# Performance work log

Hardware: AMD Instinct MI355X
Metric: run time of the kernel (lower is better)

## Reference

```python
import jax, jax.numpy as jnp
import numpy as np

B, T, E = 2, 2048, 2048
H, HKV, M = 16, 4, 4
HD = E // H // M          # 32
NREP = H // HKV           # 4
EPS = 1e-5


def _rotary_interleaved(x, cos, sin):
    # x: (B, S, nh, HD); cos/sin: (S, HD//2), interleaved pairs (0::2, 1::2)
    x1 = x[..., 0::2]
    x2 = x[..., 1::2]
    c = cos[None, :, None, :]
    s = sin[None, :, None, :]
    o1 = x1 * c - x2 * s
    o2 = x1 * s + x2 * c
    return jnp.stack([o1, o2], axis=-1).reshape(x.shape)


def setup_inputs() -> dict:
    key = jax.random.key(0)
    ks = jax.random.split(key, 6)
    x = jax.random.normal(ks[0], (B, T, E), jnp.float32)
    pos = jnp.arange(T, dtype=jnp.float32)
    inv_freq = 1.0 / (10000.0 ** (jnp.arange(0, HD, 2, dtype=jnp.float32) / HD))
    ang = pos[:, None] * inv_freq[None, :]  # (T, HD//2)
    cos = jnp.cos(ang)
    sin = jnp.sin(ang)
    s = 0.02
    q_w = jax.random.normal(ks[1], (E, E), jnp.float32) * s
    k_w = jax.random.normal(ks[2], (E // NREP, E), jnp.float32) * s
    v_w = jax.random.normal(ks[3], (E // NREP, E), jnp.float32) * s
    out_w = jax.random.normal(ks[4], (E, E), jnp.float32) * s
    raw_map_weights = jnp.array([0.1 * (-1.0) ** i for i in range(M)], jnp.float32)
    weight_scale = jnp.ones((1,), jnp.float32)
    gamma = jnp.ones((M * HD,), jnp.float32)
    return dict(x=x, cos=cos, sin=sin, q_w=q_w, k_w=k_w, v_w=v_w, out_w=out_w,
                raw_map_weights=raw_map_weights, weight_scale=weight_scale, gamma=gamma)


def reference(x, cos, sin, q_w, k_w, v_w, out_w, raw_map_weights, weight_scale, gamma):
    # projections
    q = (x @ q_w.T).reshape(B, T, M * H, HD)
    k = (x @ k_w.T).reshape(B, T, M * HKV, HD)
    v = (x @ v_w.T).reshape(B, T, HKV, M * HD)
    # rotary (interleaved) on full head_dim, then split heads x maps (heads major, maps minor)
    q = _rotary_interleaved(q, cos, sin).reshape(B, T, H, M, HD)
    k = _rotary_interleaved(k, cos, sin).reshape(B, T, HKV, M, HD)
    # GQA: q head h attends to kv head h // NREP  (repeat_interleave semantics)
    k_rep = jnp.repeat(k, NREP, axis=2)  # (B,T,H,M,HD)
    v_rep = jnp.repeat(v, NREP, axis=2)  # (B,T,H,M*HD)
    map_w = jnp.tanh(raw_map_weights) * weight_scale[0]
    scale = HD ** -0.5  # flash_attn default softmax scale
    causal = jnp.tril(jnp.ones((T, T), dtype=bool))
    combined = jnp.zeros((B, T, H, M * HD), x.dtype)
    for i in range(M):  # small fixed num_maps loop
        scores = jnp.einsum('bqhd,bkhd->bhqk', q[:, :, :, i], k_rep[:, :, :, i]) * scale
        scores = jnp.where(causal[None, None], scores, -jnp.inf)
        p = jax.nn.softmax(scores, axis=-1)
        attn_i = jnp.einsum('bhqk,bkhe->bqhe', p, v_rep)  # (B,T,H,M*HD)
        combined = combined + map_w[i] * attn_i
    # RMSNorm over last dim (num_maps * head_dim) with affine weight
    var = jnp.mean(combined * combined, axis=-1, keepdims=True)
    normed = combined * jax.lax.rsqrt(var + EPS) * gamma
    out = normed.reshape(B, T, E) @ out_w.T
    return out
```

## Files before the change

### kernel.cpp

```cpp
#include <hip/hip_runtime.h>


typedef unsigned short u16;
typedef unsigned int u32;
typedef _Float16 f16;
typedef _Float16 f16x8 __attribute__((ext_vector_type(8)));
typedef float f32x4 __attribute__((ext_vector_type(4)));

#define B_ 2
#define T_ 2048
#define E_ 2048
#define H_ 16
#define HKV_ 4
#define M_ 4
#define HD_ 32
#define SCALE_Q 0.2550348873f

#define GLOAD_LDS(g, l)                                                   \
  __builtin_amdgcn_global_load_lds(                                       \
      (const __attribute__((address_space(1))) u32*)(g),                  \
      (__attribute__((address_space(3))) u32*)(l), 16, 0, 0)

__device__ __forceinline__ u16 f2h(float f) {
  f16 h = (f16)f;
  return __builtin_bit_cast(u16, h);
}

__global__ void cvt_all(const float* __restrict__ x, const float* __restrict__ qw,
                        const float* __restrict__ kw, const float* __restrict__ vw,
                        const float* __restrict__ ow, u16* __restrict__ xb,
                        u16* __restrict__ wcat, u16* __restrict__ wo16) {
  const float* src;
  u16* dst;
  int n4;
  switch (blockIdx.y) {
    case 0: src = x;  dst = xb;            n4 = 2097152; break;
    case 1: src = qw; dst = wcat;          n4 = 1048576; break;
    case 2: src = kw; dst = wcat + 4194304; n4 = 262144; break;
    case 3: src = vw; dst = wcat + 5242880; n4 = 262144; break;
    default: src = ow; dst = wo16;         n4 = 1048576; break;
  }
  int i = blockIdx.x * blockDim.x + threadIdx.x;
  if (i < n4) {
    float4 v = ((const float4*)src)[i];
    ushort4 o;
    o.x = f2h(v.x); o.y = f2h(v.y); o.z = f2h(v.z); o.w = f2h(v.w);
    ((ushort4*)dst)[i] = o;
  }
}

#define GEMM_CORE(A_, B_ptr, K_)                                              \
  for (int k0 = 0; k0 < (K_); k0 += 32) {                                     \
    _Pragma("unroll") for (int j = 0; j < 2; ++j) {                           \
      GLOAD_LDS(&(A_)[(size_t)(m0 + r0 + j * 64) * (K_) + k0 + c8],           \
                &As[tid * 8 + j * 2048]);                                     \
      GLOAD_LDS(&(B_ptr)[(size_t)(n0 + r0 + j * 64) * (K_) + k0 + c8],        \
                &Bs[tid * 8 + j * 2048]);                                     \
    }                                                                         \
    __syncthreads();                                                          \
    f16x8 af[4], bfr[4];                                                      \
    _Pragma("unroll") for (int mt = 0; mt < 4; ++mt)                          \
        af[mt] = *(const f16x8*)&As[(wm + mt * 16 + r) * 32 + g * 8];         \
    _Pragma("unroll") for (int nt = 0; nt < 4; ++nt)                          \
        bfr[nt] = *(const f16x8*)&Bs[(wn + nt * 16 + r) * 32 + g * 8];        \
    _Pragma("unroll") for (int mt = 0; mt < 4; ++mt)                          \
        _Pragma("unroll") for (int nt = 0; nt < 4; ++nt)                      \
            acc[mt][nt] = __builtin_amdgcn_mfma_f32_16x16x32_f16(             \
                af[mt], bfr[nt], acc[mt][nt], 0, 0, 0);                       \
    __syncthreads();                                                          \
  }

__global__ __launch_bounds__(256) void gemm_bt(const u16* __restrict__ A,
                                               const u16* __restrict__ Bm,
                                               float* __restrict__ C,
                                               int M, int N, int K) {
  __shared__ __align__(16) u16 As[128 * 32];
  __shared__ __align__(16) u16 Bs[128 * 32];
  const int tid = threadIdx.x;
  const int lane = tid & 63;
  const int wv = tid >> 6;
  const int g = lane >> 4;
  const int r = lane & 15;
  const int m0 = blockIdx.y * 128;
  const int n0 = blockIdx.x * 128;
  const int wm = (wv >> 1) * 64;
  const int wn = (wv & 1) * 64;
  f32x4 acc[4][4];
#pragma unroll
  for (int a = 0; a < 4; ++a)
#pragma unroll
    for (int b = 0; b < 4; ++b) acc[a][b] = (f32x4){0.f, 0.f, 0.f, 0.f};
  const int r0 = tid >> 2;
  const int c8 = (tid & 3) << 3;

  GEMM_CORE(A, Bm, K)

#pragma unroll
  for (int mt = 0; mt < 4; ++mt)
#pragma unroll
    for (int nt = 0; nt < 4; ++nt) {
      int row = m0 + wm + mt * 16 + g * 4;
      int col = n0 + wn + nt * 16 + r;
#pragma unroll
      for (int rr = 0; rr < 4; ++rr)
        C[(size_t)(row + rr) * N + col] = acc[mt][nt][rr];
    }
}

__global__ __launch_bounds__(256) void gemm_qkv_rope(
    const u16* __restrict__ A, const u16* __restrict__ Bm,
    const float* __restrict__ cosb, const float* __restrict__ sinb,
    u16* __restrict__ qp, u16* __restrict__ kp, u16* __restrict__ vtp) {
  __shared__ __align__(16) u16 As[128 * 32];
  __shared__ __align__(16) u16 Bs[128 * 32];
  const int tid = threadIdx.x;
  const int lane = tid & 63;
  const int wv = tid >> 6;
  const int g = lane >> 4;
  const int r = lane & 15;
  const int m0 = blockIdx.y * 128;
  const int n0 = blockIdx.x * 128;
  const int wm = (wv >> 1) * 64;
  const int wn = (wv & 1) * 64;
  f32x4 acc[4][4];
#pragma unroll
  for (int a = 0; a < 4; ++a)
#pragma unroll
    for (int b = 0; b < 4; ++b) acc[a][b] = (f32x4){0.f, 0.f, 0.f, 0.f};
  const int r0 = tid >> 2;
  const int c8 = (tid & 3) << 3;

  GEMM_CORE(A, Bm, 2048)

  const int b = m0 >> 11;
  const float signf = (r & 1) ? 1.f : -1.f;
  const int jb = r >> 1;

  if (n0 < 2048) {
#pragma unroll
    for (int mt = 0; mt < 4; ++mt) {
      int row = m0 + wm + mt * 16 + g * 4;
      int t0 = row & 2047;
#pragma unroll
      for (int rr = 0; rr < 4; ++rr) {
        int t = t0 + rr;
        float c0 = cosb[t * 16 + jb], s0 = sinb[t * 16 + jb];
        float c1 = cosb[t * 16 + 8 + jb], s1 = sinb[t * 16 + 8 + jb];
#pragma unroll
        for (int nt = 0; nt < 4; ++nt) {
          float xv = acc[mt][nt][rr];
          float pv = __shfl_xor(xv, 1, 64);
          float c = (nt & 1) ? c1 : c0;
          float s = (nt & 1) ? s1 : s0;
          float o = (xv * c + signf * pv * s) * SCALE_Q;
          int col = n0 + wn + nt * 16 + r;
          int hh = col >> 7, mm = (col >> 5) & 3, d = col & 31;
          qp[((((size_t)b * H_ + hh) * M_ + mm) * T_ + t) * HD_ + d] = f2h(o);
        }
      }
    }
  } else if (n0 < 2560) {
#pragma unroll
    for (int mt = 0; mt < 4; ++mt) {
      int row = m0 + wm + mt * 16 + g * 4;
      int t0 = row & 2047;
#pragma unroll
      for (int rr = 0; rr < 4; ++rr) {
        int t = t0 + rr;
        float c0 = cosb[t * 16 + jb], s0 = sinb[t * 16 + jb];
        float c1 = cosb[t * 16 + 8 + jb], s1 = sinb[t * 16 + 8 + jb];
#pragma unroll
        for (int nt = 0; nt < 4; ++nt) {
          float xv = acc[mt][nt][rr];
          float pv = __shfl_xor(xv, 1, 64);
          float c = (nt & 1) ? c1 : c0;
          float s = (nt & 1) ? s1 : s0;
          float o = xv * c + signf * pv * s;
          int col2 = n0 + wn + nt * 16 + r - 2048;
          int hh = col2 >> 7, mm = (col2 >> 5) & 3, d = col2 & 31;
          kp[((((size_t)b * HKV_ + hh) * M_ + mm) * T_ + t) * HD_ + d] = f2h(o);
        }
      }
    }
  } else {
#pragma unroll
    for (int mt = 0; mt < 4; ++mt) {
      int row = m0 + wm + mt * 16 + g * 4;
      int t0 = row & 2047;
#pragma unroll
      for (int nt = 0; nt < 4; ++nt) {
        int col3 = n0 + wn + nt * 16 + r - 2560;
        int hkv = col3 >> 7, e = col3 & 127;
        ushort4 w;
        w.x = f2h(acc[mt][nt][0]);
        w.y = f2h(acc[mt][nt][1]);
        w.z = f2h(acc[mt][nt][2]);
        w.w = f2h(acc[mt][nt][3]);
        *(ushort4*)&vtp[(((size_t)b * HKV_ + hkv) * 128 + e) * T_ + t0] = w;
      }
    }
  }
}

__global__ __launch_bounds__(256) void lstats_kernel(
    const u16* __restrict__ qp, const u16* __restrict__ kp,
    const float* __restrict__ rawW, const float* __restrict__ wscale,
    float* __restrict__ invw) {
  const int tid = threadIdx.x;
  const int lane = tid & 63;
  const int wv = tid >> 6;
  const int g = lane >> 4, r = lane & 15;
  const int h = blockIdx.y;
  const int b = blockIdx.z >> 2, e = blockIdx.z & 3;
  const int hkv = h >> 2;
  const int s0 = blockIdx.x * 4 + wv;

  const size_t qb = (((size_t)b * H_ + h) * M_ + e) * T_ * HD_;
  const size_t kb = (((size_t)b * HKV_ + hkv) * M_ + e) * T_ * HD_;
  const float mw = tanhf(rawW[e]) * wscale[0];

  for (int ps = 0; ps < 2; ++ps) {
    const int strip = ps ? 127 - s0 : s0;
    const int q0 = strip * 16;
    f16x8 qf = *(const f16x8*)&qp[qb + (size_t)(q0 + r) * HD_ + g * 8];
    float lacc[4] = {0.f, 0.f, 0.f, 0.f};

    for (int k0 = 0; k0 < q0 + 16; k0 += 64) {
      f32x4 s[4];
#pragma unroll
      for (int nt = 0; nt < 4; ++nt) {
        f16x8 kf = *(const f16x8*)&kp[kb + (size_t)(k0 + nt * 16 + r) * HD_ + g * 8];
        s[nt] = __builtin_amdgcn_mfma_f32_16x16x32_f16(qf, kf, (f32x4){0.f, 0.f, 0.f, 0.f}, 0, 0, 0);
      }
#pragma unroll
      for (int rr = 0; rr < 4; ++rr) {
        int row = q0 + g * 4 + rr;
#pragma unroll
        for (int nt = 0; nt < 4; ++nt) {
          int col = k0 + nt * 16 + r;
          float sv = (col <= row) ? s[nt][rr] : -1e30f;
          lacc[rr] += exp2f(sv);
        }
      }
    }
#pragma unroll
    for (int rr = 0; rr < 4; ++rr) {
      float l = lacc[rr];
#pragma unroll
      for (int off = 8; off >= 1; off >>= 1) l += __shfl_xor(l, off, 64);
      if (r == 0)
        invw[(((size_t)b * H_ + h) * M_ + e) * T_ + q0 + g * 4 + rr] = mw / l;
    }
  }
}

__global__ __launch_bounds__(256) void attn_kernel(
    const u16* __restrict__ qp, const u16* __restrict__ kp,
    const u16* __restrict__ vtp, const float* __restrict__ invw,
    const float* __restrict__ gamma, u16* __restrict__ normed) {
  __shared__ __align__(16) char smem[42240];
  u16* Ks = (u16*)smem;
  u16* Pc = (u16*)(smem + 32768);
  float* comb = (float*)smem;

  const int tid = threadIdx.x;
  const int lane = tid & 63;
  const int wv = tid >> 6;
  const int g = lane >> 4;
  const int r = lane & 15;
  const int h = blockIdx.y;
  const int b = blockIdx.z;
  const int hkv = h >> 2;

  const size_t qb = ((size_t)b * H_ + h) * M_ * T_ * HD_;
  const size_t kb = ((size_t)b * HKV_ + hkv) * M_ * T_ * HD_;
  const size_t vb = ((size_t)b * HKV_ + hkv) * 128 * (size_t)T_;

#define STAGE_KS(K0, DST)                                                     \
  {                                                                           \
    _Pragma("unroll") for (int j = 0; j < 4; ++j) {                           \
      int f = tid + j * 256;                                                  \
      int e_ = f >> 8, g2 = (f >> 6) & 3, kk = f & 63;                        \
      GLOAD_LDS(&kp[kb + ((size_t)e_ * T_ + (K0) + kk) * HD_ + g2 * 8],       \
                &(DST)[f * 8]);                                               \
    }                                                                         \
  }

  for (int ps = 0; ps < 2; ++ps) {
    const int q0 = (ps ? 31 - blockIdx.x : blockIdx.x) * 64;
    const int rq = q0 + wv * 16;

    f16x8 qf[4];
    float iw[4][4];
#pragma unroll
    for (int e = 0; e < 4; ++e) {
      qf[e] = *(const f16x8*)&qp[qb + ((size_t)e * T_ + rq + r) * HD_ + g * 8];
      const float* ivp = invw + (((size_t)b * H_ + h) * M_ + e) * T_;
#pragma unroll
      for (int rr = 0; rr < 4; ++rr) iw[e][rr] = ivp[rq + g * 4 + rr];
    }

    f32x4 acc[4][2];
#pragma unroll
    for (int mt = 0; mt < 4; ++mt)
#pragma unroll
      for (int v2 = 0; v2 < 2; ++v2) acc[mt][v2] = (f32x4){0.f, 0.f, 0.f, 0.f};

    __syncthreads();
    STAGE_KS(0, (u16*)smem);
    __syncthreads();

    const int niter = q0 / 64 + 1;
    for (int i = 0; i < niter; ++i) {
      const int k0 = i * 64;
      u16* kbuf = (u16*)smem + (size_t)(i & 1) * 8192;
      u16* knext = (u16*)smem + (size_t)((i + 1) & 1) * 8192;

      if (i + 1 < niter) STAGE_KS(k0 + 64, knext);

      f16x8 vf[2][2];
#pragma unroll
      for (int v2 = 0; v2 < 2; ++v2)
#pragma unroll
        for (int k2 = 0; k2 < 2; ++k2)
          vf[v2][k2] = *(const f16x8*)&vtp[vb + (size_t)(wv * 32 + v2 * 16 + r) * T_ + k0 + k2 * 32 + g * 8];

      float pc[4][4];
#pragma unroll
      for (int nt = 0; nt < 4; ++nt)
#pragma unroll
        for (int rr = 0; rr < 4; ++rr) pc[nt][rr] = 0.f;
      if (k0 <= rq + 15) {
        const bool need_mask = (k0 + 63 > rq);
#pragma unroll
        for (int e = 0; e < 4; ++e) {
          f32x4 s[4];
#pragma unroll
          for (int nt = 0; nt < 4; ++nt) {
            f16x8 kf = *(const f16x8*)&kbuf[e * 2048 + g * 512 + (nt * 16 + r) * 8];
            s[nt] = __builtin_amdgcn_mfma_f32_16x16x32_f16(qf[e], kf, (f32x4){0.f, 0.f, 0.f, 0.f}, 0, 0, 0);
          }
#pragma unroll
          for (int nt = 0; nt < 4; ++nt)
#pragma unroll
            for (int rr = 0; rr < 4; ++rr) {
              float sv = s[nt][rr];
              if (need_mask && (k0 + nt * 16 + r > rq + g * 4 + rr)) sv = -1e30f;
              pc[nt][rr] = fmaf(exp2f(sv), iw[e][rr], pc[nt][rr]);
            }
        }
      }

      __syncthreads();

#pragma unroll
      for (int nt = 0; nt < 4; ++nt)
#pragma unroll
        for (int rr = 0; rr < 4; ++rr)
          Pc[(wv * 16 + g * 4 + rr) * 72 + nt * 16 + r] = f2h(pc[nt][rr]);

      __syncthreads();

#pragma unroll
      for (int mt = 0; mt < 4; ++mt) {
        f16x8 pf0 = *(const f16x8*)&Pc[(mt * 16 + r) * 72 + g * 8];
        f16x8 pf1 = *(const f16x8*)&Pc[(mt * 16 + r) * 72 + 32 + g * 8];
#pragma unroll
        for (int v2 = 0; v2 < 2; ++v2) {
          acc[mt][v2] = __builtin_amdgcn_mfma_f32_16x16x32_f16(pf0, vf[v2][0], acc[mt][v2], 0, 0, 0);
          acc[mt][v2] = __builtin_amdgcn_mfma_f32_16x16x32_f16(pf1, vf[v2][1], acc[mt][v2], 0, 0, 0);
        }
      }
    }

    __syncthreads();
#pragma unroll
    for (int mt = 0; mt < 4; ++mt)
#pragma unroll
      for (int v2 = 0; v2 < 2; ++v2)
#pragma unroll
        for (int rr = 0; rr < 4; ++rr)
          comb[(mt * 16 + g * 4 + rr) * 132 + wv * 32 + v2 * 16 + r] = acc[mt][v2][rr];
    __syncthreads();

    {
      int row = tid >> 2;
      int ch = (tid & 3) * 32;
      float vals[32];
      float ss = 0.f;
#pragma unroll
      for (int e2 = 0; e2 < 32; ++e2) {
        float v = comb[row * 132 + ch + e2];
        vals[e2] = v;
        ss += v * v;
      }
      ss += __shfl_xor(ss, 1, 64);
      ss += __shfl_xor(ss, 2, 64);
      float rstd = rsqrtf(ss * (1.f / 128.f) + 1e-5f);
      size_t obase = ((size_t)b * T_ + q0 + row) * E_ + (size_t)h * 128 + ch;
      union { u16 u[32]; uint4 q[4]; } pk;
#pragma unroll
      for (int e2 = 0; e2 < 32; ++e2)
        pk.u[e2] = f2h(vals[e2] * rstd * gamma[ch + e2]);
#pragma unroll
      for (int qq = 0; qq < 4; ++qq)
        *(uint4*)&normed[obase + qq * 8] = pk.q[qq];
    }
  }
#undef STAGE_KS
}

extern "C" void kernel_launch(void* const* d_in, const int* in_sizes, int n_in,
                              void* d_out, int out_size, void* d_ws, size_t ws_size,
                              hipStream_t stream) {
  const float* x = (const float*)d_in[0];
  const float* cosb = (const float*)d_in[1];
  const float* sinb = (const float*)d_in[2];
  const float* qw = (const float*)d_in[3];
  const float* kw = (const float*)d_in[4];
  const float* vw = (const float*)d_in[5];
  const float* ow = (const float*)d_in[6];
  const float* rawW = (const float*)d_in[7];
  const float* wsc = (const float*)d_in[8];
  const float* gm = (const float*)d_in[9];
  float* out = (float*)d_out;

  char* ws = (char*)d_ws;
  u16* xb = (u16*)(ws);
  u16* wcat = (u16*)(ws + (16ull << 20));
  u16* wo16 = (u16*)(ws + (28ull << 20));
  float* invw = (float*)(ws + (36ull << 20));
  u16* qp = (u16*)(ws + (84ull << 20));
  u16* kp = (u16*)(ws + (100ull << 20));
  u16* vtp = (u16*)(ws + (104ull << 20));
  u16* normed = xb;

  cvt_all<<<dim3(8192, 5), 256, 0, stream>>>(x, qw, kw, vw, ow, xb, wcat, wo16);
  gemm_qkv_rope<<<dim3(24, 32), 256, 0, stream>>>(xb, wcat, cosb, sinb, qp, kp, vtp);
  lstats_kernel<<<dim3(16, H_, B_ * M_), 256, 0, stream>>>(qp, kp, rawW, wsc, invw);
  attn_kernel<<<dim3(16, H_, B_), 256, 0, stream>>>(qp, kp, vtp, invw, gm, normed);
  gemm_bt<<<dim3(2048 / 128, 4096 / 128), 256, 0, stream>>>(normed, wo16, out, 4096, 2048, 2048);
}
```

Before: 481.9 us.

## Make each wave own its query rows for PV to drop a barrier per tile

Changes the P·V work split so each wave multiplies its own 16 query rows against all 128 value columns, rather than 64 rows against 32 columns. Each wave now writes and reads back only its own P slice, so one of the two per-iteration block barriers goes away, along with the final barrier before the combine store. The cost is that every wave loads the full V tile from global memory (four times the V traffic) and holds 8 accumulators plus 16 V fragments in registers, which raises register pressure. The per-wave causal skip is also removed, so waves whose rows are fully masked still compute scores.

```diff
diff --git a/kernel.cpp b/kernel.cpp
--- a/kernel.cpp
+++ b/kernel.cpp
@@ -258,7 +258,7 @@
     const u16* __restrict__ qp, const u16* __restrict__ kp,
     const u16* __restrict__ vtp, const float* __restrict__ invw,
     const float* __restrict__ gamma, u16* __restrict__ normed) {
-  __shared__ __align__(16) char smem[42240];
+  __shared__ __align__(16) char smem[41984];
   u16* Ks = (u16*)smem;
   u16* Pc = (u16*)(smem + 32768);
   float* comb = (float*)smem;
@@ -300,87 +300,77 @@
       for (int rr = 0; rr < 4; ++rr) iw[e][rr] = ivp[rq + g * 4 + rr];
     }
 
-    f32x4 acc[4][2];
-#pragma unroll
-    for (int mt = 0; mt < 4; ++mt)
-#pragma unroll
-      for (int v2 = 0; v2 < 2; ++v2) acc[mt][v2] = (f32x4){0.f, 0.f, 0.f, 0.f};
+    f32x4 acc[8];
+#pragma unroll
+    for (int ct = 0; ct < 8; ++ct) acc[ct] = (f32x4){0.f, 0.f, 0.f, 0.f};
 
     __syncthreads();
-    STAGE_KS(0, (u16*)smem);
+    STAGE_KS(0, Ks);
     __syncthreads();
 
     const int niter = q0 / 64 + 1;
     for (int i = 0; i < niter; ++i) {
       const int k0 = i * 64;
-      u16* kbuf = (u16*)smem + (size_t)(i & 1) * 8192;
-      u16* knext = (u16*)smem + (size_t)((i + 1) & 1) * 8192;
-
-      if (i + 1 < niter) STAGE_KS(k0 + 64, knext);
-
-      f16x8 vf[2][2];
-#pragma unroll
-      for (int v2 = 0; v2 < 2; ++v2)
+      u16* kbuf = Ks + (size_t)(i & 1) * 8192;
+      if (i + 1 < niter) STAGE_KS(k0 + 64, Ks + (size_t)((i + 1) & 1) * 8192);
+
+      f16x8 vf[2][8];
+#pragma unroll
+      for (int ct = 0; ct < 8; ++ct)
 #pragma unroll
         for (int k2 = 0; k2 < 2; ++k2)
-          vf[v2][k2] = *(const f16x8*)&vtp[vb + (size_t)(wv * 32 + v2 * 16 + r) * T_ + k0 + k2 * 32 + g * 8];
+          vf[k2][ct] = *(const f16x8*)&vtp[vb + (size_t)(ct * 16 + r) * T_ + k0 + k2 * 32 + g * 8];
 
       float pc[4][4];
 #pragma unroll
       for (int nt = 0; nt < 4; ++nt)
 #pragma unroll
         for (int rr = 0; rr < 4; ++rr) pc[nt][rr] = 0.f;
-      if (k0 <= rq + 15) {
-        const bool need_mask = (k0 + 63 > rq);
-#pragma unroll
-        for (int e = 0; e < 4; ++e) {
-          f32x4 s[4];
-#pragma unroll
-          for (int nt = 0; nt < 4; ++nt) {
-            f16x8 kf = *(const f16x8*)&kbuf[e * 2048 + g * 512 + (nt * 16 + r) * 8];
-            s[nt] = __builtin_amdgcn_mfma_f32_16x16x32_f16(qf[e], kf, (f32x4){0.f, 0.f, 0.f, 0.f}, 0, 0, 0);
+      const bool need_mask = (k0 + 63 > rq);
+#pragma unroll
+      for (int e = 0; e < 4; ++e) {
+        f32x4 s[4];
+#pragma unroll
+        for (int nt = 0; nt < 4; ++nt) {
+          f16x8 kf = *(const f16x8*)&kbuf[e * 2048 + g * 512 + (nt * 16 + r) * 8];
+          s[nt] = __builtin_amdgcn_mfma_f32_16x16x32_f16(qf[e], kf, (f32x4){0.f, 0.f, 0.f, 0.f}, 0, 0, 0);
+        }
+#pragma unroll
+        for (int nt = 0; nt < 4; ++nt)
+#pragma unroll
+          for (int rr = 0; rr < 4; ++rr) {
+            float sv = s[nt][rr];
+            if (need_mask && (k0 + nt * 16 + r > rq + g * 4 + rr)) sv = -1e30f;
+            pc[nt][rr] = fmaf(exp2f(sv), iw[e][rr], pc[nt][rr]);
           }
-#pragma unroll
-          for (int nt = 0; nt < 4; ++nt)
-#pragma unroll
-            for (int rr = 0; rr < 4; ++rr) {
-              float sv = s[nt][rr];
-              if (need_mask && (k0 + nt * 16 + r > rq + g * 4 + rr)) sv = -1e30f;
-              pc[nt][rr] = fmaf(exp2f(sv), iw[e][rr], pc[nt][rr]);
-            }
-        }
+      }
+
+      u16* myP = Pc + wv * (16 * 72);
+#pragma unroll
+      for (int nt = 0; nt < 4; ++nt)
+#pragma unroll
+        for (int rr = 0; rr < 4; ++rr)
+          myP[(g * 4 + rr) * 72 + nt * 16 + r] = f2h(pc[nt][rr]);
+
+      f16x8 pf[2];
+#pragma unroll
+      for (int k2 = 0; k2 < 2; ++k2)
+        pf[k2] = *(const f16x8*)&myP[r * 72 + k2 * 32 + g * 8];
+
+#pragma unroll
+      for (int ct = 0; ct < 8; ++ct) {
+        acc[ct] = __builtin_amdgcn_mfma_f32_16x16x32_f16(pf[0], vf[0][ct], acc[ct], 0, 0, 0);
+        acc[ct] = __builtin_amdgcn_mfma_f32_16x16x32_f16(pf[1], vf[1][ct], acc[ct], 0, 0, 0);
       }
 
       __syncthreads();
-
-#pragma unroll
-      for (int nt = 0; nt < 4; ++nt)
-#pragma unroll
-        for (int rr = 0; rr < 4; ++rr)
-          Pc[(wv * 16 + g * 4 + rr) * 72 + nt * 16 + r] = f2h(pc[nt][rr]);
-
-      __syncthreads();
-
-#pragma unroll
-      for (int mt = 0; mt < 4; ++mt) {
-        f16x8 pf0 = *(const f16x8*)&Pc[(mt * 16 + r) * 72 + g * 8];
-        f16x8 pf1 = *(const f16x8*)&Pc[(mt * 16 + r) * 72 + 32 + g * 8];
-#pragma unroll
-        for (int v2 = 0; v2 < 2; ++v2) {
-          acc[mt][v2] = __builtin_amdgcn_mfma_f32_16x16x32_f16(pf0, vf[v2][0], acc[mt][v2], 0, 0, 0);
-          acc[mt][v2] = __builtin_amdgcn_mfma_f32_16x16x32_f16(pf1, vf[v2][1], acc[mt][v2], 0, 0, 0);
-        }
-      }
-    }
-
-    __syncthreads();
-#pragma unroll
-    for (int mt = 0; mt < 4; ++mt)
-#pragma unroll
-      for (int v2 = 0; v2 < 2; ++v2)
-#pragma unroll
-        for (int rr = 0; rr < 4; ++rr)
-          comb[(mt * 16 + g * 4 + rr) * 132 + wv * 32 + v2 * 16 + r] = acc[mt][v2][rr];
+    }
+
+#pragma unroll
+    for (int ct = 0; ct < 8; ++ct)
+#pragma unroll
+      for (int rr = 0; rr < 4; ++rr)
+        comb[(wv * 16 + g * 4 + rr) * 132 + ct * 16 + r] = acc[ct][rr];
     __syncthreads();
 
     {
```

Result: slower. 515.7 us (+7.0%).

## Shrink attention tile to 32 query rows with two waves and single K buffer

Applied to the files above, without the earlier changes.

The attention kernel now uses 128-thread blocks, each handling 32 query rows instead of 64, so twice as many blocks are launched. Each wave now covers 64 of the V columns in the PV product. The double-buffered K staging becomes a single buffer that is refilled after the score pass, which roughly halves LDS use. The aim is better occupancy and load balance across CUs. In exchange, each K and V tile is reused by fewer query rows, which raises global and LDS traffic, and K loads are no longer overlapped with score compute.

```diff
diff --git a/kernel.cpp b/kernel.cpp
--- a/kernel.cpp
+++ b/kernel.cpp
@@ -254,13 +254,13 @@
   }
 }
 
-__global__ __launch_bounds__(256) void attn_kernel(
+__global__ __launch_bounds__(128) void attn_kernel(
     const u16* __restrict__ qp, const u16* __restrict__ kp,
     const u16* __restrict__ vtp, const float* __restrict__ invw,
     const float* __restrict__ gamma, u16* __restrict__ normed) {
-  __shared__ __align__(16) char smem[42240];
+  __shared__ __align__(16) char smem[20992];
   u16* Ks = (u16*)smem;
-  u16* Pc = (u16*)(smem + 32768);
+  u16* Pc = (u16*)(smem + 16384);
   float* comb = (float*)smem;
 
   const int tid = threadIdx.x;
@@ -276,18 +276,18 @@
   const size_t kb = ((size_t)b * HKV_ + hkv) * M_ * T_ * HD_;
   const size_t vb = ((size_t)b * HKV_ + hkv) * 128 * (size_t)T_;
 
-#define STAGE_KS(K0, DST)                                                     \
+#define STAGE_KS(K0)                                                          \
   {                                                                           \
-    _Pragma("unroll") for (int j = 0; j < 4; ++j) {                           \
-      int f = tid + j * 256;                                                  \
+    _Pragma("unroll") for (int j = 0; j < 8; ++j) {                           \
+      int f = tid + j * 128;                                                  \
       int e_ = f >> 8, g2 = (f >> 6) & 3, kk = f & 63;                        \
       GLOAD_LDS(&kp[kb + ((size_t)e_ * T_ + (K0) + kk) * HD_ + g2 * 8],       \
-                &(DST)[f * 8]);                                               \
+                &Ks[f * 8]);                                                  \
     }                                                                         \
   }
 
   for (int ps = 0; ps < 2; ++ps) {
-    const int q0 = (ps ? 31 - blockIdx.x : blockIdx.x) * 64;
+    const int q0 = (ps ? 63 - blockIdx.x : blockIdx.x) * 32;
     const int rq = q0 + wv * 16;
 
     f16x8 qf[4];
@@ -300,55 +300,49 @@
       for (int rr = 0; rr < 4; ++rr) iw[e][rr] = ivp[rq + g * 4 + rr];
     }
 
-    f32x4 acc[4][2];
-#pragma unroll
-    for (int mt = 0; mt < 4; ++mt)
-#pragma unroll
-      for (int v2 = 0; v2 < 2; ++v2) acc[mt][v2] = (f32x4){0.f, 0.f, 0.f, 0.f};
+    f32x4 acc[2][4];
+#pragma unroll
+    for (int mt = 0; mt < 2; ++mt)
+#pragma unroll
+      for (int ct = 0; ct < 4; ++ct) acc[mt][ct] = (f32x4){0.f, 0.f, 0.f, 0.f};
 
     __syncthreads();
-    STAGE_KS(0, (u16*)smem);
+    STAGE_KS(0);
     __syncthreads();
 
     const int niter = q0 / 64 + 1;
     for (int i = 0; i < niter; ++i) {
       const int k0 = i * 64;
-      u16* kbuf = (u16*)smem + (size_t)(i & 1) * 8192;
-      u16* knext = (u16*)smem + (size_t)((i + 1) & 1) * 8192;
-
-      if (i + 1 < niter) STAGE_KS(k0 + 64, knext);
-
-      f16x8 vf[2][2];
-#pragma unroll
-      for (int v2 = 0; v2 < 2; ++v2)
+
+      f16x8 vf[2][4];
+#pragma unroll
+      for (int ct = 0; ct < 4; ++ct)
 #pragma unroll
         for (int k2 = 0; k2 < 2; ++k2)
-          vf[v2][k2] = *(const f16x8*)&vtp[vb + (size_t)(wv * 32 + v2 * 16 + r) * T_ + k0 + k2 * 32 + g * 8];
+          vf[k2][ct] = *(const f16x8*)&vtp[vb + (size_t)(wv * 64 + ct * 16 + r) * T_ + k0 + k2 * 32 + g * 8];
 
       float pc[4][4];
 #pragma unroll
       for (int nt = 0; nt < 4; ++nt)
 #pragma unroll
         for (int rr = 0; rr < 4; ++rr) pc[nt][rr] = 0.f;
-      if (k0 <= rq + 15) {
-        const bool need_mask = (k0 + 63 > rq);
-#pragma unroll
-        for (int e = 0; e < 4; ++e) {
-          f32x4 s[4];
-#pragma unroll
-          for (int nt = 0; nt < 4; ++nt) {
-            f16x8 kf = *(const f16x8*)&kbuf[e * 2048 + g * 512 + (nt * 16 + r) * 8];
-            s[nt] = __builtin_amdgcn_mfma_f32_16x16x32_f16(qf[e], kf, (f32x4){0.f, 0.f, 0.f, 0.f}, 0, 0, 0);
+      const bool need_mask = (k0 + 63 > rq);
+#pragma unroll
+      for (int e = 0; e < 4; ++e) {
+        f32x4 s[4];
+#pragma unroll
+        for (int nt = 0; nt < 4; ++nt) {
+          f16x8 kf = *(const f16x8*)&Ks[e * 2048 + g * 512 + (nt * 16 + r) * 8];
+          s[nt] = __builtin_amdgcn_mfma_f32_16x16x32_f16(qf[e], kf, (f32x4){0.f, 0.f, 0.f, 0.f}, 0, 0, 0);
+        }
+#pragma unroll
+        for (int nt = 0; nt < 4; ++nt)
+#pragma unroll
+          for (int rr = 0; rr < 4; ++rr) {
+            float sv = s[nt][rr];
+            if (need_mask && (k0 + nt * 16 + r > rq + g * 4 + rr)) sv = -1e30f;
+            pc[nt][rr] = fmaf(exp2f(sv), iw[e][rr], pc[nt][rr]);
           }
-#pragma unroll
-          for (int nt = 0; nt < 4; ++nt)
-#pragma unroll
-            for (int rr = 0; rr < 4; ++rr) {
-              float sv = s[nt][rr];
-              if (need_mask && (k0 + nt * 16 + r > rq + g * 4 + rr)) sv = -1e30f;
-              pc[nt][rr] = fmaf(exp2f(sv), iw[e][rr], pc[nt][rr]);
-            }
-        }
       }
 
       __syncthreads();
@@ -359,28 +353,30 @@
         for (int rr = 0; rr < 4; ++rr)
           Pc[(wv * 16 + g * 4 + rr) * 72 + nt * 16 + r] = f2h(pc[nt][rr]);
 
+      if (i + 1 < niter) STAGE_KS(k0 + 64);
+
       __syncthreads();
 
 #pragma unroll
-      for (int mt = 0; mt < 4; ++mt) {
+      for (int mt = 0; mt < 2; ++mt) {
         f16x8 pf0 = *(const f16x8*)&Pc[(mt * 16 + r) * 72 + g * 8];
         f16x8 pf1 = *(const f16x8*)&Pc[(mt * 16 + r) * 72 + 32 + g * 8];
 #pragma unroll
-        for (int v2 = 0; v2 < 2; ++v2) {
-          acc[mt][v2] = __builtin_amdgcn_mfma_f32_16x16x32_f16(pf0, vf[v2][0], acc[mt][v2], 0, 0, 0);
-          acc[mt][v2] = __builtin_amdgcn_mfma_f32_16x16x32_f16(pf1, vf[v2][1], acc[mt][v2], 0, 0, 0);
+        for (int ct = 0; ct < 4; ++ct) {
+          acc[mt][ct] = __builtin_amdgcn_mfma_f32_16x16x32_f16(pf0, vf[0][ct], acc[mt][ct], 0, 0, 0);
+          acc[mt][ct] = __builtin_amdgcn_mfma_f32_16x16x32_f16(pf1, vf[1][ct], acc[mt][ct], 0, 0, 0);
         }
       }
     }
 
     __syncthreads();
 #pragma unroll
-    for (int mt = 0; mt < 4; ++mt)
-#pragma unroll
-      for (int v2 = 0; v2 < 2; ++v2)
+    for (int mt = 0; mt < 2; ++mt)
+#pragma unroll
+      for (int ct = 0; ct < 4; ++ct)
 #pragma unroll
         for (int rr = 0; rr < 4; ++rr)
-          comb[(mt * 16 + g * 4 + rr) * 132 + wv * 32 + v2 * 16 + r] = acc[mt][v2][rr];
+          comb[(mt * 16 + g * 4 + rr) * 132 + wv * 64 + ct * 16 + r] = acc[mt][ct][rr];
     __syncthreads();
 
     {
@@ -438,6 +434,6 @@
   cvt_all<<<dim3(8192, 5), 256, 0, stream>>>(x, qw, kw, vw, ow, xb, wcat, wo16);
   gemm_qkv_rope<<<dim3(24, 32), 256, 0, stream>>>(xb, wcat, cosb, sinb, qp, kp, vtp);
   lstats_kernel<<<dim3(16, H_, B_ * M_), 256, 0, stream>>>(qp, kp, rawW, wsc, invw);
-  attn_kernel<<<dim3(16, H_, B_), 256, 0, stream>>>(qp, kp, vtp, invw, gm, normed);
+  attn_kernel<<<dim3(32, H_, B_), 128, 0, stream>>>(qp, kp, vtp, invw, gm, normed);
   gemm_bt<<<dim3(2048 / 128, 4096 / 128), 256, 0, stream>>>(normed, wo16, out, 4096, 2048, 2048);
 }
```

Measured after the change: 479.8 us. About the same (-0.4%).
